# Kernel tuning notes

Hardware: AMD Instinct MI355X
Metric: run time of the kernel (lower is better)

Reference implementation:

```python
import jax, jax.numpy as jnp
import numpy as np

B, S1, S2, D, H, FFN = 4, 1024, 1024, 1024, 16, 4096
DK = D // H  # 64
EPS = 1e-5


def layer_norm(x, g, b):
    m = jnp.mean(x, axis=-1, keepdims=True)
    v = jnp.mean((x - m) ** 2, axis=-1, keepdims=True)
    return (x - m) * jax.lax.rsqrt(v + EPS) * g + b


def cross_attention(y, kvn, mask, qw, kw, vw, ow, ob):
    # y: [B,S1,D], kvn: [B,S2,D], mask: [B,S2] int (0 -> masked)
    q = (y @ qw).reshape(B, S1, H, DK)
    k = (kvn @ kw).reshape(B, S2, H, DK)
    v = (kvn @ vw).reshape(B, S2, H, DK)
    attn = jnp.einsum('bqhd,bkhd->bhqk', q, k) / np.sqrt(DK).astype(np.float32)
    attn = jnp.where(mask[:, None, None, :] == 0, jnp.float32(-1e9), attn)
    attn = jax.nn.softmax(attn, axis=-1)
    out = jnp.einsum('bhqk,bkhd->bqhd', attn, v).reshape(B, S1, H * DK)
    return out @ ow + ob


def setup_inputs() -> dict:
    key = jax.random.key(0)
    ks = jax.random.split(key, 16)
    s = 1.0 / np.sqrt(D)
    inp = {
        'x': jax.random.normal(ks[0], (B, S1, D), jnp.float32),
        'kv': jax.random.normal(ks[1], (B, S2, D), jnp.float32),
        'attn_bias': jax.random.randint(ks[2], (B, S2), 0, 2, jnp.int32),
        'ln1_g': jnp.ones((D,), jnp.float32),
        'ln1_b': jnp.zeros((D,), jnp.float32),
        'qw0': jax.random.normal(ks[3], (D, D), jnp.float32) * s,
        'kw0': jax.random.normal(ks[4], (D, D), jnp.float32) * s,
        'vw0': jax.random.normal(ks[5], (D, D), jnp.float32) * s,
        'ow0': jax.random.normal(ks[6], (D, D), jnp.float32) * s,
        'ob0': jnp.zeros((D,), jnp.float32),
        'qw1': jax.random.normal(ks[7], (D, D), jnp.float32) * s,
        'kw1': jax.random.normal(ks[8], (D, D), jnp.float32) * s,
        'vw1': jax.random.normal(ks[9], (D, D), jnp.float32) * s,
        'ow1': jax.random.normal(ks[10], (D, D), jnp.float32) * s,
        'ob1': jnp.zeros((D,), jnp.float32),
        'ln2_g': jnp.ones((D,), jnp.float32),
        'ln2_b': jnp.zeros((D,), jnp.float32),
        'w1': jax.random.normal(ks[11], (D, FFN), jnp.float32) * s,
        'b1': jnp.zeros((FFN,), jnp.float32),
        'w2': jax.random.normal(ks[12], (FFN, D), jnp.float32) * (1.0 / np.sqrt(FFN)),
        'b2': jnp.zeros((D,), jnp.float32),
    }
    return inp


def reference(x, kv, attn_bias, ln1_g, ln1_b, qw0, kw0, vw0, ow0, ob0,
              qw1, kw1, vw1, ow1, ob1, ln2_g, ln2_b, w1, b1, w2, b2):
    y = layer_norm(x, ln1_g, ln1_b)
    kvn = layer_norm(kv, ln1_g, ln1_b)  # same norm module applied to both
    y = cross_attention(y, kvn, attn_bias, qw0, kw0, vw0, ow0, ob0) + y
    y = cross_attention(y, kvn, attn_bias, qw1, kw1, vw1, ow1, ob1) + y
    x = x + y  # dropout rate 0 -> identity
    y = layer_norm(x, ln2_g, ln2_b)
    y = jax.nn.relu(y @ w1 + b1) @ w2 + b2
    x = x + y
    return x
```

## Files before the change

kernel.cpp:

```cpp
#include <hip/hip_runtime.h>
#include <stdint.h>

typedef unsigned short u16;
typedef __bf16 bf16x8 __attribute__((ext_vector_type(8)));
typedef float f32x4 __attribute__((ext_vector_type(4)));

#define LOG2E 1.4426950408889634f

__device__ __forceinline__ float bf2f(u16 a) {
  union { unsigned u; float f; } v; v.u = ((unsigned)a) << 16; return v.f;
}
__device__ __forceinline__ u16 f2bf(float f) {
  union { float f; unsigned u; } v; v.f = f;
  unsigned r = v.u + 0x7fffu + ((v.u >> 16) & 1u);
  return (u16)(r >> 16);
}
__device__ __forceinline__ void gl_lds16(const void* g, void* l) {
  __builtin_amdgcn_global_load_lds(
      (const __attribute__((address_space(1))) uint32_t*)g,
      (__attribute__((address_space(3))) uint32_t*)l,
      16, 0, 0);
}

__device__ __forceinline__ int swz(int row, int colu16) {
  return row * 64 + (colu16 ^ (((row ^ (row >> 2)) & 7) << 3));
}

template <int BM, int BN, int MODE>
__global__ __launch_bounds__(256) void gemm_bt(
    const u16* __restrict__ A, const u16* __restrict__ Bt,
    u16* Cbf, float* C32,
    const float* __restrict__ bias,
    const u16* resbf, const float* __restrict__ resx,
    int M, int N, int K)
{
  constexpr int MT = BM / 32, NT = BN / 32;
  constexpr int GA = (BM * 4) / 256, GB = (BN * 4) / 256;
  __shared__ u16 sA[BM * 32];
  __shared__ u16 sB[BN * 32];
  const int tid  = threadIdx.x;
  const int wave = tid >> 6, lane = tid & 63;
  const int quad = lane >> 4, l16 = lane & 15;
  const int wm = wave >> 1, wn = wave & 1;
  const int m0 = blockIdx.y * BM, n0 = blockIdx.x * BN;

  f32x4 acc[MT][NT] = {};

  for (int k0 = 0; k0 < K; k0 += 32) {
    __syncthreads();
#pragma unroll
    for (int i = 0; i < GA; ++i) {
      int cb = i * 256 + wave * 64;
      int c = cb + lane;
      int row = c >> 2, kc = c & 3;
      gl_lds16(A + (size_t)(m0 + row) * K + k0 + kc * 8, &sA[cb * 8]);
    }
#pragma unroll
    for (int i = 0; i < GB; ++i) {
      int cb = i * 256 + wave * 64;
      int c = cb + lane;
      int row = c >> 2, kc = c & 3;
      gl_lds16(Bt + (size_t)(n0 + row) * K + k0 + kc * 8, &sB[cb * 8]);
    }
    __syncthreads();

    bf16x8 fa[MT], fb[NT];
#pragma unroll
    for (int mt = 0; mt < MT; ++mt)
      fa[mt] = *(const bf16x8*)&sA[(wm * (BM / 2) + mt * 16 + l16) * 32 + quad * 8];
#pragma unroll
    for (int nt = 0; nt < NT; ++nt)
      fb[nt] = *(const bf16x8*)&sB[(wn * (BN / 2) + nt * 16 + l16) * 32 + quad * 8];
#pragma unroll
    for (int mt = 0; mt < MT; ++mt)
#pragma unroll
      for (int nt = 0; nt < NT; ++nt)
        acc[mt][nt] = __builtin_amdgcn_mfma_f32_16x16x32_bf16(
            fa[mt], fb[nt], acc[mt][nt], 0, 0, 0);
  }

#pragma unroll
  for (int mt = 0; mt < MT; ++mt) {
#pragma unroll
    for (int nt = 0; nt < NT; ++nt) {
#pragma unroll
      for (int r = 0; r < 4; ++r) {
        int row = m0 + wm * (BM / 2) + mt * 16 + quad * 4 + r;
        int col = n0 + wn * (BN / 2) + nt * 16 + l16;
        size_t idx = (size_t)row * N + col;
        float v = acc[mt][nt][r];
        if constexpr (MODE == 0) {
          Cbf[idx] = f2bf(v);
        } else if constexpr (MODE == 1) {
          v += bias[col] + bf2f(resbf[idx]);
          Cbf[idx] = f2bf(v);
        } else if constexpr (MODE == 2) {
          v = fmaxf(v + bias[col], 0.f);
          Cbf[idx] = f2bf(v);
        } else if constexpr (MODE == 3) {
          v += bias[col] + resx[idx] + bf2f(resbf[idx]);
          C32[idx] = v;
        } else {
          C32[idx] = C32[idx] + v;
        }
      }
    }
  }
}

__global__ __launch_bounds__(256) void transpose64(
    const float* __restrict__ in, u16* __restrict__ out, int R, int Cstride)
{
  __shared__ u16 tile[64][72];
  const int r0 = blockIdx.y * 64, c0 = blockIdx.x * 64;
  const int t = threadIdx.x;
  {
    const int lr = t >> 4, lc = (t & 15) * 4;
#pragma unroll
    for (int h = 0; h < 4; ++h) {
      int row = h * 16 + lr;
      float4 vd = *(const float4*)&in[(size_t)(r0 + row) * Cstride + c0 + lc];
      ushort4 ov;
      ov.x = f2bf(vd.x); ov.y = f2bf(vd.y); ov.z = f2bf(vd.z); ov.w = f2bf(vd.w);
      *(ushort4*)&tile[row][lc] = ov;
    }
  }
  __syncthreads();
  {
    const int lr = t >> 3, lv = t & 7;
#pragma unroll
    for (int h = 0; h < 2; ++h) {
      int orow = h * 32 + lr;
      u16 tmp[8];
#pragma unroll
      for (int j = 0; j < 8; ++j) tmp[j] = tile[lv * 8 + j][orow];
      *(uint4*)&out[(size_t)(c0 + orow) * R + r0 + lv * 8] = *(uint4*)tmp;
    }
  }
}

__global__ __launch_bounds__(256) void vt_kernel(
    const u16* __restrict__ in, u16* __restrict__ out)
{
  __shared__ u16 tile[64][72];
  const int st = blockIdx.x, bh = blockIdx.y;
  const int b = bh >> 4, h = bh & 15;
  const int t = threadIdx.x;
  const int lr = t >> 3, lv = t & 7;
  const u16* src = in + ((size_t)b * 1024 + st * 64) * 2048 + 1024 + h * 64;
#pragma unroll
  for (int half = 0; half < 2; ++half) {
    int row = half * 32 + lr;
    uint4 vd = *(const uint4*)&src[(size_t)row * 2048 + lv * 8];
    *(uint4*)&tile[row][lv * 8] = vd;
  }
  __syncthreads();
  u16* dst = out + (size_t)bh * 64 * 1024 + st * 64;
#pragma unroll
  for (int half = 0; half < 2; ++half) {
    int orow = half * 32 + lr;
    u16 tmp[8];
#pragma unroll
    for (int j = 0; j < 8; ++j) tmp[j] = tile[lv * 8 + j][orow];
    *(uint4*)&dst[(size_t)orow * 1024 + lv * 8] = *(uint4*)tmp;
  }
}

__global__ __launch_bounds__(256) void ln_kernel(
    const float* __restrict__ x, const float* __restrict__ g,
    const float* __restrict__ b, u16* __restrict__ outbf)
{
  const int row = blockIdx.x, t = threadIdx.x;
  const int wave = t >> 6, lane = t & 63;
  float4 xv = *(const float4*)&x[(size_t)row * 1024 + t * 4];
  float v0 = xv.x, v1 = xv.y, v2 = xv.z, v3 = xv.w;
  float s = v0 + v1 + v2 + v3;
  float s2 = v0 * v0 + v1 * v1 + v2 * v2 + v3 * v3;
  for (int m = 1; m < 64; m <<= 1) { s += __shfl_xor(s, m); s2 += __shfl_xor(s2, m); }
  __shared__ float ps[4], pq[4];
  if (lane == 0) { ps[wave] = s; pq[wave] = s2; }
  __syncthreads();
  s = ps[0] + ps[1] + ps[2] + ps[3];
  s2 = pq[0] + pq[1] + pq[2] + pq[3];
  float mean = s * (1.f / 1024.f);
  float var = s2 * (1.f / 1024.f) - mean * mean;
  float rs = rsqrtf(var + 1e-5f);
  float4 gv = *(const float4*)&g[t * 4];
  float4 bv = *(const float4*)&b[t * 4];
  ushort4 ov;
  ov.x = f2bf((v0 - mean) * rs * gv.x + bv.x);
  ov.y = f2bf((v1 - mean) * rs * gv.y + bv.y);
  ov.z = f2bf((v2 - mean) * rs * gv.z + bv.z);
  ov.w = f2bf((v3 - mean) * rs * gv.w + bv.w);
  *(ushort4*)&outbf[(size_t)row * 1024 + t * 4] = ov;
}

__global__ __launch_bounds__(256) void ln_add_kernel(
    const float* __restrict__ x, const u16* __restrict__ ybf,
    const float* __restrict__ g, const float* __restrict__ b,
    u16* __restrict__ hbf)
{
  const int row = blockIdx.x, t = threadIdx.x;
  const int wave = t >> 6, lane = t & 63;
  float4 xv = *(const float4*)&x[(size_t)row * 1024 + t * 4];
  ushort4 yv = *(const ushort4*)&ybf[(size_t)row * 1024 + t * 4];
  float v0 = xv.x + bf2f(yv.x), v1 = xv.y + bf2f(yv.y);
  float v2 = xv.z + bf2f(yv.z), v3 = xv.w + bf2f(yv.w);
  float s = v0 + v1 + v2 + v3;
  float s2 = v0 * v0 + v1 * v1 + v2 * v2 + v3 * v3;
  for (int m = 1; m < 64; m <<= 1) { s += __shfl_xor(s, m); s2 += __shfl_xor(s2, m); }
  __shared__ float ps[4], pq[4];
  if (lane == 0) { ps[wave] = s; pq[wave] = s2; }
  __syncthreads();
  s = ps[0] + ps[1] + ps[2] + ps[3];
  s2 = pq[0] + pq[1] + pq[2] + pq[3];
  float mean = s * (1.f / 1024.f);
  float var = s2 * (1.f / 1024.f) - mean * mean;
  float rs = rsqrtf(var + 1e-5f);
  float4 gv = *(const float4*)&g[t * 4];
  float4 bv = *(const float4*)&b[t * 4];
  ushort4 ov;
  ov.x = f2bf((v0 - mean) * rs * gv.x + bv.x);
  ov.y = f2bf((v1 - mean) * rs * gv.y + bv.y);
  ov.z = f2bf((v2 - mean) * rs * gv.z + bv.z);
  ov.w = f2bf((v3 - mean) * rs * gv.w + bv.w);
  *(ushort4*)&hbf[(size_t)row * 1024 + t * 4] = ov;
}

__global__ __launch_bounds__(256) void attn_kernel(
    const u16* __restrict__ Q,
    const u16* __restrict__ K,
    const u16* __restrict__ Vt,
    const int* __restrict__ mask,
    u16* __restrict__ O)
{
  __shared__ u16 sK[64 * 64], sVt[64 * 64], sP[64 * 64];
  __shared__ float smaskf[64];
  const int qt = blockIdx.x, h = blockIdx.y, b = blockIdx.z;
  const int t = threadIdx.x;
  const int wave = t >> 6, lane = t & 63;
  const int quad = lane >> 4, l16 = lane & 15;
  const u16* Qb = Q + (size_t)b * 1024 * 1024 + (size_t)qt * 64 * 1024 + h * 64;
  const u16* Kb = K + (size_t)b * 1024 * 2048 + h * 64;
  const u16* Vb = Vt + (size_t)(b * 16 + h) * 64 * 1024;

#pragma unroll
  for (int i = 0; i < 2; ++i) {
    int cb = i * 256 + wave * 64;
    int c = cb + lane;
    int row = c >> 3;
    int scc = (c & 7) ^ ((row ^ (row >> 2)) & 7);
    gl_lds16(Qb + (size_t)row * 1024 + scc * 8, &sP[cb * 8]);
  }
  __syncthreads();
  bf16x8 aq[2];
#pragma unroll
  for (int ks = 0; ks < 2; ++ks)
    aq[ks] = *(const bf16x8*)&sP[swz(wave * 16 + l16, ks * 32 + quad * 8)];

  float m2_[4], l_[4];
  f32x4 accO[4] = {};
#pragma unroll
  for (int r = 0; r < 4; ++r) { m2_[r] = -1e30f; l_[r] = 0.f; }

  constexpr float QS = 0.125f * LOG2E;

  for (int j = 0; j < 16; ++j) {
    __syncthreads();
#pragma unroll
    for (int i = 0; i < 2; ++i) {
      int cb = i * 256 + wave * 64;
      int c = cb + lane;
      int row = c >> 3;
      int scc = (c & 7) ^ ((row ^ (row >> 2)) & 7);
      gl_lds16(Kb + (size_t)(j * 64 + row) * 2048 + scc * 8, &sK[cb * 8]);
      gl_lds16(Vb + (size_t)row * 1024 + j * 64 + scc * 8, &sVt[cb * 8]);
    }
    if (t < 64) smaskf[t] = (mask[b * 1024 + j * 64 + t] == 0) ? -1e9f : 0.f;
    __syncthreads();

    f32x4 accS[4] = {};
#pragma unroll
    for (int ks = 0; ks < 2; ++ks) {
#pragma unroll
      for (int nt = 0; nt < 4; ++nt) {
        bf16x8 bk = *(const bf16x8*)&sK[swz(nt * 16 + l16, ks * 32 + quad * 8)];
        accS[nt] = __builtin_amdgcn_mfma_f32_16x16x32_bf16(aq[ks], bk, accS[nt], 0, 0, 0);
      }
    }
    float mf[4];
#pragma unroll
    for (int nt = 0; nt < 4; ++nt) mf[nt] = smaskf[nt * 16 + l16];

#pragma unroll
    for (int r = 0; r < 4; ++r) {
      float v0 = fmaf(accS[0][r], QS, mf[0]);
      float v1 = fmaf(accS[1][r], QS, mf[1]);
      float v2 = fmaf(accS[2][r], QS, mf[2]);
      float v3 = fmaf(accS[3][r], QS, mf[3]);
      float cm = fmaxf(fmaxf(v0, v1), fmaxf(v2, v3));
      for (int sh = 1; sh < 16; sh <<= 1) cm = fmaxf(cm, __shfl_xor(cm, sh));
      float nm = fmaxf(m2_[r], cm);
      float alpha = exp2f(m2_[r] - nm);
      m2_[r] = nm;
      float p0 = exp2f(v0 - nm), p1 = exp2f(v1 - nm);
      float p2 = exp2f(v2 - nm), p3 = exp2f(v3 - nm);
      l_[r] = l_[r] * alpha + (p0 + p1 + p2 + p3);
      int prow = wave * 16 + quad * 4 + r;
      sP[swz(prow, 0 * 16 + l16)] = f2bf(p0);
      sP[swz(prow, 1 * 16 + l16)] = f2bf(p1);
      sP[swz(prow, 2 * 16 + l16)] = f2bf(p2);
      sP[swz(prow, 3 * 16 + l16)] = f2bf(p3);
#pragma unroll
      for (int nt2 = 0; nt2 < 4; ++nt2) accO[nt2][r] *= alpha;
    }
    __syncthreads();
#pragma unroll
    for (int ks = 0; ks < 2; ++ks) {
      bf16x8 ap = *(const bf16x8*)&sP[swz(wave * 16 + l16, ks * 32 + quad * 8)];
#pragma unroll
      for (int nt2 = 0; nt2 < 4; ++nt2) {
        bf16x8 bvv = *(const bf16x8*)&sVt[swz(nt2 * 16 + l16, ks * 32 + quad * 8)];
        accO[nt2] = __builtin_amdgcn_mfma_f32_16x16x32_bf16(ap, bvv, accO[nt2], 0, 0, 0);
      }
    }
  }

  u16* Ob = O + (size_t)b * 1024 * 1024 + (size_t)qt * 64 * 1024 + h * 64;
#pragma unroll
  for (int r = 0; r < 4; ++r) {
    float lr = l_[r];
    for (int sh = 1; sh < 16; sh <<= 1) lr += __shfl_xor(lr, sh);
    float inv = 1.f / lr;
    int row = wave * 16 + quad * 4 + r;
#pragma unroll
    for (int nt2 = 0; nt2 < 4; ++nt2)
      Ob[(size_t)row * 1024 + nt2 * 16 + l16] = f2bf(accO[nt2][r] * inv);
  }
}

extern "C" void kernel_launch(void* const* d_in, const int* in_sizes, int n_in,
                              void* d_out, int out_size, void* d_ws, size_t ws_size,
                              hipStream_t stream)
{
  const float* x   = (const float*)d_in[0];
  const float* kv  = (const float*)d_in[1];
  const int* attn_bias = (const int*)d_in[2];
  const float* ln1_g = (const float*)d_in[3];
  const float* ln1_b = (const float*)d_in[4];
  const float* qw0 = (const float*)d_in[5];
  const float* kw0 = (const float*)d_in[6];
  const float* vw0 = (const float*)d_in[7];
  const float* ow0 = (const float*)d_in[8];
  const float* ob0 = (const float*)d_in[9];
  const float* qw1 = (const float*)d_in[10];
  const float* kw1 = (const float*)d_in[11];
  const float* vw1 = (const float*)d_in[12];
  const float* ow1 = (const float*)d_in[13];
  const float* ob1 = (const float*)d_in[14];
  const float* ln2_g = (const float*)d_in[15];
  const float* ln2_b = (const float*)d_in[16];
  const float* w1 = (const float*)d_in[17];
  const float* b1 = (const float*)d_in[18];
  const float* w2 = (const float*)d_in[19];
  const float* b2 = (const float*)d_in[20];

  char* ws = (char*)d_ws;
  const size_t MB = 1u << 20;
  u16* Wkv   = (u16*)(ws + 0 * MB);
  u16* Wsm   = (u16*)(ws + 4 * MB);
  u16* wtA   = (u16*)(ws + 0 * MB);
  u16* wtB   = (u16*)(ws + 4 * MB);
  u16* ybf   = (u16*)(ws + 8 * MB);
  u16* kvnbf = (u16*)(ws + 16 * MB);
  u16* qbuf  = (u16*)(ws + 24 * MB);
  u16* kvbuf = (u16*)(ws + 32 * MB);
  u16* hbf   = kvnbf;
  u16* fbuf  = kvbuf;
  u16* attnb = (u16*)d_out;
  u16* vT    = (u16*)((char*)d_out + 8 * MB);
  float* out32 = (float*)d_out;

  const dim3 B256(256);
  const dim3 gT(16, 16);
  const dim3 gGemmN1k(8, 64);
  const dim3 gGemm2k(16, 32);
  const dim3 gVt(16, 64);
  const dim3 gAttn(16, 16, 4);

  ln_kernel<<<4096, B256, 0, stream>>>(x,  ln1_g, ln1_b, ybf);
  ln_kernel<<<4096, B256, 0, stream>>>(kv, ln1_g, ln1_b, kvnbf);

  for (int layer = 0; layer < 2; ++layer) {
    const float* qw = layer ? qw1 : qw0;
    const float* kw = layer ? kw1 : kw0;
    const float* vw = layer ? vw1 : vw0;
    const float* ow = layer ? ow1 : ow0;
    const float* ob = layer ? ob1 : ob0;

    transpose64<<<gT, B256, 0, stream>>>(kw, Wkv, 1024, 1024);
    transpose64<<<gT, B256, 0, stream>>>(vw, Wkv + 1024 * 1024, 1024, 1024);
    gemm_bt<128, 128, 0><<<gGemm2k, B256, 0, stream>>>(
        kvnbf, Wkv, kvbuf, nullptr, nullptr, nullptr, nullptr, 4096, 2048, 1024);
    transpose64<<<gT, B256, 0, stream>>>(qw, Wsm, 1024, 1024);
    gemm_bt<64, 128, 0><<<gGemmN1k, B256, 0, stream>>>(
        ybf, Wsm, qbuf, nullptr, nullptr, nullptr, nullptr, 4096, 1024, 1024);
    vt_kernel<<<gVt, B256, 0, stream>>>(kvbuf, vT);

    attn_kernel<<<gAttn, B256, 0, stream>>>(qbuf, kvbuf, vT, attn_bias, attnb);

    transpose64<<<gT, B256, 0, stream>>>(ow, Wsm, 1024, 1024);
    gemm_bt<64, 128, 1><<<gGemmN1k, B256, 0, stream>>>(
        attnb, Wsm, ybf, nullptr, ob, ybf, nullptr, 4096, 1024, 1024);
  }

  ln_add_kernel<<<4096, B256, 0, stream>>>(x, ybf, ln2_g, ln2_b, hbf);

  for (int band = 0; band < 2; ++band) {
    transpose64<<<dim3(32, 16), B256, 0, stream>>>(w1 + band * 2048, wtA, 1024, 4096);
    transpose64<<<dim3(16, 32), B256, 0, stream>>>(w2 + (size_t)band * 2048 * 1024,
                                                   wtB, 2048, 1024);
    gemm_bt<128, 128, 2><<<gGemm2k, B256, 0, stream>>>(
        hbf, wtA, fbuf, nullptr, b1 + band * 2048, nullptr, nullptr,
        4096, 2048, 1024);
    if (band == 0) {
      gemm_bt<64, 128, 3><<<gGemmN1k, B256, 0, stream>>>(
          fbuf, wtB, nullptr, out32, b2, ybf, x, 4096, 1024, 2048);
    } else {
      gemm_bt<64, 128, 4><<<gGemmN1k, B256, 0, stream>>>(
          fbuf, wtB, nullptr, out32, nullptr, nullptr, nullptr, 4096, 1024, 2048);
    }
  }
}
```

Before: 648.1 us.

## Double-buffer attention K/V tiles, lazy softmax rescale, widen GEMM K-step

```diff
diff --git a/kernel.cpp b/kernel.cpp
--- a/kernel.cpp
+++ b/kernel.cpp
@@ -14,6 +14,10 @@
   union { float f; unsigned u; } v; v.f = f;
   unsigned r = v.u + 0x7fffu + ((v.u >> 16) & 1u);
   return (u16)(r >> 16);
+}
+__device__ __forceinline__ u16 f2bf_fast(float f) {
+  __bf16 h = (__bf16)f;
+  union { __bf16 h; u16 u; } v; v.h = h; return v.u;
 }
 __device__ __forceinline__ void gl_lds16(const void* g, void* l) {
   __builtin_amdgcn_global_load_lds(
@@ -35,9 +39,9 @@
     int M, int N, int K)
 {
   constexpr int MT = BM / 32, NT = BN / 32;
-  constexpr int GA = (BM * 4) / 256, GB = (BN * 4) / 256;
-  __shared__ u16 sA[BM * 32];
-  __shared__ u16 sB[BN * 32];
+  constexpr int GA = BM / 32, GB = BN / 32;
+  __shared__ u16 sA[BM * 64];
+  __shared__ u16 sB[BN * 64];
   const int tid  = threadIdx.x;
   const int wave = tid >> 6, lane = tid & 63;
   const int quad = lane >> 4, l16 = lane & 15;
@@ -46,37 +50,40 @@
 
   f32x4 acc[MT][NT] = {};
 
-  for (int k0 = 0; k0 < K; k0 += 32) {
+  for (int k0 = 0; k0 < K; k0 += 64) {
     __syncthreads();
 #pragma unroll
     for (int i = 0; i < GA; ++i) {
       int cb = i * 256 + wave * 64;
       int c = cb + lane;
-      int row = c >> 2, kc = c & 3;
+      int row = c >> 3, kc = c & 7;
       gl_lds16(A + (size_t)(m0 + row) * K + k0 + kc * 8, &sA[cb * 8]);
     }
 #pragma unroll
     for (int i = 0; i < GB; ++i) {
       int cb = i * 256 + wave * 64;
       int c = cb + lane;
-      int row = c >> 2, kc = c & 3;
+      int row = c >> 3, kc = c & 7;
       gl_lds16(Bt + (size_t)(n0 + row) * K + k0 + kc * 8, &sB[cb * 8]);
     }
     __syncthreads();
 
-    bf16x8 fa[MT], fb[NT];
-#pragma unroll
-    for (int mt = 0; mt < MT; ++mt)
-      fa[mt] = *(const bf16x8*)&sA[(wm * (BM / 2) + mt * 16 + l16) * 32 + quad * 8];
-#pragma unroll
-    for (int nt = 0; nt < NT; ++nt)
-      fb[nt] = *(const bf16x8*)&sB[(wn * (BN / 2) + nt * 16 + l16) * 32 + quad * 8];
-#pragma unroll
-    for (int mt = 0; mt < MT; ++mt)
+#pragma unroll
+    for (int kk = 0; kk < 2; ++kk) {
+      bf16x8 fa[MT], fb[NT];
+#pragma unroll
+      for (int mt = 0; mt < MT; ++mt)
+        fa[mt] = *(const bf16x8*)&sA[(wm * (BM / 2) + mt * 16 + l16) * 64 + kk * 32 + quad * 8];
 #pragma unroll
       for (int nt = 0; nt < NT; ++nt)
-        acc[mt][nt] = __builtin_amdgcn_mfma_f32_16x16x32_bf16(
-            fa[mt], fb[nt], acc[mt][nt], 0, 0, 0);
+        fb[nt] = *(const bf16x8*)&sB[(wn * (BN / 2) + nt * 16 + l16) * 64 + kk * 32 + quad * 8];
+#pragma unroll
+      for (int mt = 0; mt < MT; ++mt)
+#pragma unroll
+        for (int nt = 0; nt < NT; ++nt)
+          acc[mt][nt] = __builtin_amdgcn_mfma_f32_16x16x32_bf16(
+              fa[mt], fb[nt], acc[mt][nt], 0, 0, 0);
+    }
   }
 
 #pragma unroll
@@ -234,8 +241,7 @@
     const int* __restrict__ mask,
     u16* __restrict__ O)
 {
-  __shared__ u16 sK[64 * 64], sVt[64 * 64], sP[64 * 64];
-  __shared__ float smaskf[64];
+  __shared__ u16 sK[2][64 * 64], sVt[2][64 * 64], sP[64 * 64];
   const int qt = blockIdx.x, h = blockIdx.y, b = blockIdx.z;
   const int t = threadIdx.x;
   const int wave = t >> 6, lane = t & 63;
@@ -243,6 +249,7 @@
   const u16* Qb = Q + (size_t)b * 1024 * 1024 + (size_t)qt * 64 * 1024 + h * 64;
   const u16* Kb = K + (size_t)b * 1024 * 2048 + h * 64;
   const u16* Vb = Vt + (size_t)(b * 16 + h) * 64 * 1024;
+  const int* maskb = mask + b * 1024;
 
 #pragma unroll
   for (int i = 0; i < 2; ++i) {
@@ -251,6 +258,8 @@
     int row = c >> 3;
     int scc = (c & 7) ^ ((row ^ (row >> 2)) & 7);
     gl_lds16(Qb + (size_t)row * 1024 + scc * 8, &sP[cb * 8]);
+    gl_lds16(Kb + (size_t)row * 2048 + scc * 8, &sK[0][cb * 8]);
+    gl_lds16(Vb + (size_t)row * 1024 + scc * 8, &sVt[0][cb * 8]);
   }
   __syncthreads();
   bf16x8 aq[2];
@@ -267,61 +276,78 @@
 
   for (int j = 0; j < 16; ++j) {
     __syncthreads();
-#pragma unroll
-    for (int i = 0; i < 2; ++i) {
-      int cb = i * 256 + wave * 64;
-      int c = cb + lane;
-      int row = c >> 3;
-      int scc = (c & 7) ^ ((row ^ (row >> 2)) & 7);
-      gl_lds16(Kb + (size_t)(j * 64 + row) * 2048 + scc * 8, &sK[cb * 8]);
-      gl_lds16(Vb + (size_t)row * 1024 + j * 64 + scc * 8, &sVt[cb * 8]);
-    }
-    if (t < 64) smaskf[t] = (mask[b * 1024 + j * 64 + t] == 0) ? -1e9f : 0.f;
-    __syncthreads();
-
+    float mf[4];
+#pragma unroll
+    for (int nt = 0; nt < 4; ++nt)
+      mf[nt] = (maskb[j * 64 + nt * 16 + l16] == 0) ? -1e9f : 0.f;
+    if (j < 15) {
+      const int jn = j + 1, bs = jn & 1;
+#pragma unroll
+      for (int i = 0; i < 2; ++i) {
+        int cb = i * 256 + wave * 64;
+        int c = cb + lane;
+        int row = c >> 3;
+        int scc = (c & 7) ^ ((row ^ (row >> 2)) & 7);
+        gl_lds16(Kb + (size_t)(jn * 64 + row) * 2048 + scc * 8, &sK[bs][cb * 8]);
+        gl_lds16(Vb + (size_t)row * 1024 + jn * 64 + scc * 8, &sVt[bs][cb * 8]);
+      }
+    }
+    const u16* sKc = sK[j & 1];
     f32x4 accS[4] = {};
 #pragma unroll
     for (int ks = 0; ks < 2; ++ks) {
 #pragma unroll
       for (int nt = 0; nt < 4; ++nt) {
-        bf16x8 bk = *(const bf16x8*)&sK[swz(nt * 16 + l16, ks * 32 + quad * 8)];
+        bf16x8 bk = *(const bf16x8*)&sKc[swz(nt * 16 + l16, ks * 32 + quad * 8)];
         accS[nt] = __builtin_amdgcn_mfma_f32_16x16x32_bf16(aq[ks], bk, accS[nt], 0, 0, 0);
       }
     }
-    float mf[4];
-#pragma unroll
-    for (int nt = 0; nt < 4; ++nt) mf[nt] = smaskf[nt * 16 + l16];
-
+    float vv[4][4], cm_[4];
+    bool need = false;
 #pragma unroll
     for (int r = 0; r < 4; ++r) {
-      float v0 = fmaf(accS[0][r], QS, mf[0]);
-      float v1 = fmaf(accS[1][r], QS, mf[1]);
-      float v2 = fmaf(accS[2][r], QS, mf[2]);
-      float v3 = fmaf(accS[3][r], QS, mf[3]);
-      float cm = fmaxf(fmaxf(v0, v1), fmaxf(v2, v3));
+#pragma unroll
+      for (int nt = 0; nt < 4; ++nt) vv[r][nt] = fmaf(accS[nt][r], QS, mf[nt]);
+      float cm = fmaxf(fmaxf(vv[r][0], vv[r][1]), fmaxf(vv[r][2], vv[r][3]));
       for (int sh = 1; sh < 16; sh <<= 1) cm = fmaxf(cm, __shfl_xor(cm, sh));
-      float nm = fmaxf(m2_[r], cm);
-      float alpha = exp2f(m2_[r] - nm);
-      m2_[r] = nm;
-      float p0 = exp2f(v0 - nm), p1 = exp2f(v1 - nm);
-      float p2 = exp2f(v2 - nm), p3 = exp2f(v3 - nm);
-      l_[r] = l_[r] * alpha + (p0 + p1 + p2 + p3);
+      cm_[r] = cm;
+      need = need || (cm > m2_[r] + 8.f);
+    }
+    if (__any(need)) {
+#pragma unroll
+      for (int r = 0; r < 4; ++r) {
+        float nm = fmaxf(m2_[r], cm_[r]);
+        float al = exp2f(m2_[r] - nm);
+        m2_[r] = nm;
+        l_[r] *= al;
+#pragma unroll
+        for (int n2 = 0; n2 < 4; ++n2) accO[n2][r] *= al;
+      }
+    }
+#pragma unroll
+    for (int r = 0; r < 4; ++r) {
       int prow = wave * 16 + quad * 4 + r;
-      sP[swz(prow, 0 * 16 + l16)] = f2bf(p0);
-      sP[swz(prow, 1 * 16 + l16)] = f2bf(p1);
-      sP[swz(prow, 2 * 16 + l16)] = f2bf(p2);
-      sP[swz(prow, 3 * 16 + l16)] = f2bf(p3);
-#pragma unroll
-      for (int nt2 = 0; nt2 < 4; ++nt2) accO[nt2][r] *= alpha;
-    }
-    __syncthreads();
+      float rs = 0.f;
+#pragma unroll
+      for (int nt = 0; nt < 4; ++nt) {
+        float p = exp2f(vv[r][nt] - m2_[r]);
+        rs += p;
+        sP[swz(prow, nt * 16 + l16)] = f2bf_fast(p);
+      }
+      l_[r] += rs;
+    }
+    __builtin_amdgcn_sched_barrier(0);
+    asm volatile("s_waitcnt lgkmcnt(0)" ::: "memory");
+    __builtin_amdgcn_s_barrier();
+    __builtin_amdgcn_sched_barrier(0);
+    const u16* sVc = sVt[j & 1];
 #pragma unroll
     for (int ks = 0; ks < 2; ++ks) {
       bf16x8 ap = *(const bf16x8*)&sP[swz(wave * 16 + l16, ks * 32 + quad * 8)];
 #pragma unroll
-      for (int nt2 = 0; nt2 < 4; ++nt2) {
-        bf16x8 bvv = *(const bf16x8*)&sVt[swz(nt2 * 16 + l16, ks * 32 + quad * 8)];
-        accO[nt2] = __builtin_amdgcn_mfma_f32_16x16x32_bf16(ap, bvv, accO[nt2], 0, 0, 0);
+      for (int n2 = 0; n2 < 4; ++n2) {
+        bf16x8 bv = *(const bf16x8*)&sVc[swz(n2 * 16 + l16, ks * 32 + quad * 8)];
+        accO[n2] = __builtin_amdgcn_mfma_f32_16x16x32_bf16(ap, bv, accO[n2], 0, 0, 0);
       }
     }
   }
@@ -334,8 +360,8 @@
     float inv = 1.f / lr;
     int row = wave * 16 + quad * 4 + r;
 #pragma unroll
-    for (int nt2 = 0; nt2 < 4; ++nt2)
-      Ob[(size_t)row * 1024 + nt2 * 16 + l16] = f2bf(accO[nt2][r] * inv);
+    for (int n2 = 0; n2 < 4; ++n2)
+      Ob[(size_t)row * 1024 + n2 * 16 + l16] = f2bf_fast(accO[n2][r] * inv);
   }
 }
 
```

Result: slower. 675.6 us (+4.3%).
